# Kernel optimization log

Measured on AMD Instinct MI355X. Metric: run time of the kernel, lower is better.

Reference implementation:

```python
import jax, jax.numpy as jnp
import numpy as np

N_NODES = 100000
N_EDGES = 1200000
N_GRAPHS = 512
IN_DIM, HID, N_CLS = 16, 64, 2
EPS = 1e-5


def setup_inputs() -> dict:
    key = jax.random.key(0)
    ks = jax.random.split(key, 24)
    d = {}
    d["x"] = jax.random.normal(ks[0], (N_NODES, IN_DIM), dtype=jnp.float32)
    d["edge_index"] = jax.random.randint(ks[1], (2, N_EDGES), 0, N_NODES, dtype=jnp.int32)
    d["batch_ids"] = jnp.sort(jax.random.randint(ks[2], (N_NODES,), 0, N_GRAPHS, dtype=jnp.int32))
    # input batchnorm affine
    d["bn_in_g"] = jnp.ones((IN_DIM,), jnp.float32)
    d["bn_in_b"] = jnp.zeros((IN_DIM,), jnp.float32)
    # 3 GCN layers: weight, bias, bn gamma, bn beta
    dims = [(IN_DIM, HID), (HID, HID), (HID, HID)]
    for i, (ci, co) in enumerate(dims):
        s = 1.0 / np.sqrt(ci)
        d[f"W{i}"] = jax.random.uniform(ks[3 + 4 * i], (ci, co), jnp.float32, -s, s)
        d[f"b{i}"] = jnp.zeros((co,), jnp.float32)
        d[f"g{i}"] = jnp.ones((co,), jnp.float32)
        d[f"be{i}"] = jnp.zeros((co,), jnp.float32)
    # classifier head: Linear(HID,HID) -> ReLU -> Linear(HID,N_CLS)
    s = 1.0 / np.sqrt(HID)
    d["Wc1"] = jax.random.uniform(ks[20], (HID, HID), jnp.float32, -s, s)
    d["bc1"] = jax.random.uniform(ks[21], (HID,), jnp.float32, -s, s)
    d["Wc2"] = jax.random.uniform(ks[22], (HID, N_CLS), jnp.float32, -s, s)
    d["bc2"] = jax.random.uniform(ks[23], (N_CLS,), jnp.float32, -s, s)
    return d


def _batchnorm(x, g, b):
    # training-mode BatchNorm1d: biased batch stats over nodes
    m = jnp.mean(x, axis=0)
    v = jnp.mean(jnp.square(x - m), axis=0)
    return (x - m) * jax.lax.rsqrt(v + EPS) * g + b


def _gcn(x, W, b, src, dst, dis):
    # GCNConv: out[i] = sum_{j->i} dis[j]*dis[i] * (x_j W) + b  (self-loops included in src/dst)
    h = x @ W                                  # [N, co]
    msg = h[src] * (dis[src] * dis[dst])[:, None]  # [E+N, co] gather
    return jax.ops.segment_sum(msg, dst, num_segments=N_NODES) + b


def reference(x, bn_in_g, bn_in_b, W0, b0, g0, be0, W1, b1, g1, be1,
              W2, b2, g2, be2, Wc1, bc1, Wc2, bc2, edge_index, batch_ids):
    loops = jnp.arange(N_NODES, dtype=edge_index.dtype)
    src = jnp.concatenate([edge_index[0], loops])
    dst = jnp.concatenate([edge_index[1], loops])
    deg = jax.ops.segment_sum(jnp.ones(src.shape[0], x.dtype), dst, num_segments=N_NODES)
    dis = jnp.where(deg > 0, jax.lax.rsqrt(jnp.maximum(deg, 1e-12)), 0.0)

    h = _batchnorm(x, bn_in_g, bn_in_b)
    for W, b, g, be in ((W0, b0, g0, be0), (W1, b1, g1, be1), (W2, b2, g2, be2)):
        h = jax.nn.relu(_batchnorm(_gcn(h, W, b, src, dst, dis), g, be))

    # global mean pool over graphs
    sums = jax.ops.segment_sum(h, batch_ids, num_segments=N_GRAPHS)
    cnt = jax.ops.segment_sum(jnp.ones((N_NODES,), h.dtype), batch_ids, num_segments=N_GRAPHS)
    pooled = sums / jnp.maximum(cnt, 1.0)[:, None]

    # classifier head (dropout omitted: eval mode)
    z = jax.nn.relu(pooled @ Wc1 + bc1)
    return z @ Wc2 + bc2
```

## Files before the change

### kernel.cpp

```cpp
#include <hip/hip_runtime.h>
#include <hip/hip_bf16.h>

#define N_NODES 100000
#define N_EDGES 1200000
#define N_GRAPHS 512
#define HID 64
#define IN_DIM 16
#define EPS 1e-5f

#define NB_BUCKETS 391
#define BUCKET_SPAN 256
#define REGION 4096
#define BIN_TILE 4096
#define CSR_LEN (N_EDGES + N_NODES)
#define NREP 64
#define STATS_BLKS 64

typedef _Float16 half4 __attribute__((ext_vector_type(4)));
typedef _Float16 half8 __attribute__((ext_vector_type(8)));


__global__ void bin_stats_kernel(const int* __restrict__ ei, int* __restrict__ bucketCnt,
                                 int* __restrict__ regions, const float* __restrict__ x,
                                 float* __restrict__ sums, float* __restrict__ sumsq,
                                 _Float16* __restrict__ hwBuf, int nbBin) {
    __shared__ int hist[NB_BUCKETS], basem[NB_BUCKETS], cur[NB_BUCKETS];
    __shared__ float ls[16], lq[16];
    int t = threadIdx.x;

    if (blockIdx.x >= nbBin) {
        const int sblk = blockIdx.x - nbBin;
        if (sblk == 0 && t < 8)
            ((float4*)(hwBuf + (size_t)N_NODES * HID))[t] = make_float4(0.f, 0.f, 0.f, 0.f);
        if (t < 16) { ls[t] = 0.f; lq[t] = 0.f; }
        __syncthreads();
        const float4* x4 = (const float4*)x;
        const int total4 = N_NODES * IN_DIM / 4;
        float s0 = 0.f, s1 = 0.f, s2 = 0.f, s3 = 0.f;
        float q0 = 0.f, q1 = 0.f, q2 = 0.f, q3 = 0.f;
        int i = sblk * 256 + t;
        const int fb = (i & 3) * 4;
        for (; i < total4; i += STATS_BLKS * 256) {
            float4 v = x4[i];
            s0 += v.x; q0 += v.x * v.x;
            s1 += v.y; q1 += v.y * v.y;
            s2 += v.z; q2 += v.z * v.z;
            s3 += v.w; q3 += v.w * v.w;
        }
        atomicAdd(&ls[fb + 0], s0); atomicAdd(&lq[fb + 0], q0);
        atomicAdd(&ls[fb + 1], s1); atomicAdd(&lq[fb + 1], q1);
        atomicAdd(&ls[fb + 2], s2); atomicAdd(&lq[fb + 2], q2);
        atomicAdd(&ls[fb + 3], s3); atomicAdd(&lq[fb + 3], q3);
        __syncthreads();
        if (t < 16) { atomicAdd(&sums[t], ls[t]); atomicAdd(&sumsq[t], lq[t]); }
        return;
    }

    for (int i = t; i < NB_BUCKETS; i += 256) { hist[i] = 0; cur[i] = 0; }
    __syncthreads();
    const int4* ei4s = (const int4*)ei;
    const int4* ei4d = (const int4*)(ei + N_EDGES);
    int srcs[16], dsts[16];
#pragma unroll
    for (int i = 0; i < 4; i++) {
        int idx4 = blockIdx.x * (BIN_TILE / 4) + t + i * 256;
        if (idx4 * 4 < N_EDGES) {
            int4 s4 = ei4s[idx4];
            int4 d4 = ei4d[idx4];
            srcs[i * 4 + 0] = s4.x; dsts[i * 4 + 0] = d4.x;
            srcs[i * 4 + 1] = s4.y; dsts[i * 4 + 1] = d4.y;
            srcs[i * 4 + 2] = s4.z; dsts[i * 4 + 2] = d4.z;
            srcs[i * 4 + 3] = s4.w; dsts[i * 4 + 3] = d4.w;
            atomicAdd(&hist[d4.x >> 8], 1);
            atomicAdd(&hist[d4.y >> 8], 1);
            atomicAdd(&hist[d4.z >> 8], 1);
            atomicAdd(&hist[d4.w >> 8], 1);
        } else {
            dsts[i * 4 + 0] = -1; dsts[i * 4 + 1] = -1;
            dsts[i * 4 + 2] = -1; dsts[i * 4 + 3] = -1;
        }
    }
    __syncthreads();
    for (int i = t; i < NB_BUCKETS; i += 256) {
        int h = hist[i];
        basem[i] = h ? atomicAdd(&bucketCnt[i], h) : 0;
    }
    __syncthreads();
#pragma unroll
    for (int i = 0; i < 16; i++) {
        if (dsts[i] >= 0) {
            int b = dsts[i] >> 8;
            int pos = basem[b] + atomicAdd(&cur[b], 1);
            if (pos < REGION)
                regions[b * REGION + pos] = srcs[i] | ((dsts[i] & 255) << 17);
        }
    }
}


__global__ void build_kernel(const int* __restrict__ regions, const int* __restrict__ bucketCnt,
                             int* __restrict__ csrOff, int* __restrict__ csrSrc,
                             float* __restrict__ dis, const float* __restrict__ x,
                             const float* __restrict__ sums, const float* __restrict__ sumsq,
                             const float* __restrict__ gamma, const float* __restrict__ beta,
                             half4* __restrict__ m4) {
    __shared__ int deg[256], cur[256];
    __shared__ int slice[REGION + 256];
    __shared__ int wred1[4], wred2[4];
    __shared__ float sc16[16], sh16[16];
    int b = blockIdx.x, t = threadIdx.x;
    const int laneid = t & 63;
    const int w = t >> 6;

    if (t < 16) {
        const float invn = 1.0f / (float)N_NODES;
        float m = sums[t] * invn;
        float var = sumsq[t] * invn - m * m;
        float rs = rsqrtf(var + EPS);
        sc16[t] = gamma[t] * rs;
        sh16[t] = beta[t] - m * sc16[t];
    }
    {
        int s = 0;
        for (int i = t; i < NB_BUCKETS; i += 256)
            if (i < b) s += min(bucketCnt[i], REGION);
#pragma unroll
        for (int d = 1; d < 64; d <<= 1) s += __shfl_xor(s, d, 64);
        if (laneid == 0) wred1[w] = s;
    }
    int cnt = min(bucketCnt[b], REGION);
    int nbase = b * BUCKET_SPAN;
    int n = nbase + t;
    bool valid = (n < N_NODES);
    deg[t] = valid ? 1 : 0;
    __syncthreads();
    const int bb = wred1[0] + wred1[1] + wred1[2] + wred1[3] + b * BUCKET_SPAN;

    for (int i = t; i < cnt; i += 256) {
        int rec = regions[b * REGION + i];
        atomicAdd(&deg[rec >> 17], 1);
    }
    __syncthreads();
    int d = deg[t];

    int v = d;
#pragma unroll
    for (int sh = 1; sh < 64; sh <<= 1) {
        int u = __shfl_up(v, sh, 64);
        if (laneid >= sh) v += u;
    }
    if (laneid == 63) wred2[w] = v;
    __syncthreads();
    int wpre = 0;
#pragma unroll
    for (int ww = 0; ww < 4; ww++)
        if (ww < w) wpre += wred2[ww];
    const int tot = wred2[0] + wred2[1] + wred2[2] + wred2[3];
    int excl = v + wpre - d;

    float dv = rsqrtf((float)d);
    if (valid) {
        csrOff[n] = bb + excl;
        dis[n] = dv;
    }
    if (b == 0 && t == 0) csrOff[N_NODES] = CSR_LEN;
    cur[t] = excl;
    __syncthreads();
    if (valid) {
        int pos = atomicAdd(&cur[t], 1);
        slice[pos] = n;
    }
    for (int i = t; i < cnt; i += 256) {
        int rec = regions[b * REGION + i];
        int pos = atomicAdd(&cur[rec >> 17], 1);
        slice[pos] = rec & 0x1FFFF;
    }
    __syncthreads();
    for (int i = t; i < tot; i += 256) csrSrc[bb + i] = slice[i];

    if (valid) {
        const float4* xr = (const float4*)x + (size_t)n * 4;
        half4* mr = m4 + (size_t)n * 4;
#pragma unroll
        for (int c = 0; c < 4; c++) {
            float4 h = xr[c];
            half4 o;
            o.x = (_Float16)((h.x * sc16[c * 4 + 0] + sh16[c * 4 + 0]) * dv);
            o.y = (_Float16)((h.y * sc16[c * 4 + 1] + sh16[c * 4 + 1]) * dv);
            o.z = (_Float16)((h.z * sc16[c * 4 + 2] + sh16[c * 4 + 2]) * dv);
            o.w = (_Float16)((h.w * sc16[c * 4 + 3] + sh16[c * 4 + 3]) * dv);
            mr[c] = o;
        }
    } else if (n == N_NODES) {
        half4 z;
        z.x = (_Float16)0.f; z.y = (_Float16)0.f; z.z = (_Float16)0.f; z.w = (_Float16)0.f;
        half4* mr = m4 + (size_t)n * 4;
#pragma unroll
        for (int c = 0; c < 4; c++) mr[c] = z;
    }
}


__device__ __forceinline__ void bn_coef_rep(const float* rep, const float* gamma,
                                            const float* beta, int k, float& sc, float& sh) {
    float S = 0.f, Q = 0.f;
    for (int r = 0; r < NREP; r++) { S += rep[r * 128 + k]; Q += rep[r * 128 + 64 + k]; }
    const float invn = 1.0f / (float)N_NODES;
    float m = S * invn;
    float var = Q * invn - m * m;
    float rs = rsqrtf(var + EPS);
    sc = gamma[k] * rs;
    sh = beta[k] - m * sc;
}


__global__ void agg16_gemm0_kernel(const half4* __restrict__ m4, const int* __restrict__ csrOff,
                                   const int* __restrict__ csrSrc, const float* __restrict__ dis,
                                   const float* __restrict__ W, const float* __restrict__ bias,
                                   _Float16* __restrict__ y, float* __restrict__ statsRep) {
    const int t = threadIdx.x;
    const int lane = t & 63;
    const int wid = t >> 6;
    const int g = lane >> 4;
    const int s = lane & 15;
    const int fl = s & 3;
    const int q = s >> 2;
    const int wave = blockIdx.x * 4 + wid;
    const int nwaves = gridDim.x * 4;

    float wreg[16][4];
#pragma unroll
    for (int k = 0; k < 16; k++) {
#pragma unroll
        for (int j = 0; j < 4; j++) wreg[k][j] = W[k * HID + s + 16 * j];
    }
    float bj[4];
#pragma unroll
    for (int j = 0; j < 4; j++) bj[j] = bias[s + 16 * j];
    float sv[4] = {0.f, 0.f, 0.f, 0.f}, qv[4] = {0.f, 0.f, 0.f, 0.f};

    for (int n0 = wave * 4; n0 < N_NODES; n0 += nwaves * 4) {
        int n = n0 + g;
        bool vn = (n < N_NODES);
        int beg = 0, end = 0;
        if (vn) { beg = csrOff[n]; end = csrOff[n + 1]; }
        float4 acc = make_float4(0.f, 0.f, 0.f, 0.f);
        int e = beg + q;
        int i0 = (e < end) ? csrSrc[e] : N_NODES;
        int i1 = (e + 4 < end) ? csrSrc[e + 4] : N_NODES;
        while (e < end) {
            int j0 = i0, j1 = i1;
            e += 8;
            i0 = (e < end) ? csrSrc[e] : N_NODES;
            i1 = (e + 4 < end) ? csrSrc[e + 4] : N_NODES;
            half4 v0 = m4[(size_t)j0 * 4 + fl];
            half4 v1 = m4[(size_t)j1 * 4 + fl];
            acc.x += (float)v0.x + (float)v1.x;
            acc.y += (float)v0.y + (float)v1.y;
            acc.z += (float)v0.z + (float)v1.z;
            acc.w += (float)v0.w + (float)v1.w;
        }
        acc.x += __shfl_xor(acc.x, 4, 64);  acc.y += __shfl_xor(acc.y, 4, 64);
        acc.z += __shfl_xor(acc.z, 4, 64);  acc.w += __shfl_xor(acc.w, 4, 64);
        acc.x += __shfl_xor(acc.x, 8, 64);  acc.y += __shfl_xor(acc.y, 8, 64);
        acc.z += __shfl_xor(acc.z, 8, 64);  acc.w += __shfl_xor(acc.w, 8, 64);
        float d = vn ? dis[n] : 0.f;
        acc.x *= d; acc.y *= d; acc.z *= d; acc.w *= d;
        float yv0 = bj[0], yv1 = bj[1], yv2 = bj[2], yv3 = bj[3];
        const int gbase = lane & 48;
#pragma unroll
        for (int k = 0; k < 16; k++) {
            float comp = ((k & 3) == 0) ? acc.x : ((k & 3) == 1) ? acc.y
                        : ((k & 3) == 2) ? acc.z : acc.w;
            float a = __shfl(comp, gbase + (k >> 2), 64);
            yv0 += a * wreg[k][0];
            yv1 += a * wreg[k][1];
            yv2 += a * wreg[k][2];
            yv3 += a * wreg[k][3];
        }
        if (vn) {
            _Float16* yr = y + (size_t)n * HID;
            yr[s] = (_Float16)yv0; yr[s + 16] = (_Float16)yv1;
            yr[s + 32] = (_Float16)yv2; yr[s + 48] = (_Float16)yv3;
            sv[0] += yv0; qv[0] += yv0 * yv0;
            sv[1] += yv1; qv[1] += yv1 * yv1;
            sv[2] += yv2; qv[2] += yv2 * yv2;
            sv[3] += yv3; qv[3] += yv3 * yv3;
        }
    }
#pragma unroll
    for (int j = 0; j < 4; j++) {
        sv[j] += __shfl_xor(sv[j], 16, 64); sv[j] += __shfl_xor(sv[j], 32, 64);
        qv[j] += __shfl_xor(qv[j], 16, 64); qv[j] += __shfl_xor(qv[j], 32, 64);
    }
    __shared__ float ls[4][64], lq[4][64];
    if (g == 0) {
#pragma unroll
        for (int j = 0; j < 4; j++) { ls[wid][s + 16 * j] = sv[j]; lq[wid][s + 16 * j] = qv[j]; }
    }
    __syncthreads();
    if (wid == 0) {
        float S = ls[0][lane] + ls[1][lane] + ls[2][lane] + ls[3][lane];
        float Q = lq[0][lane] + lq[1][lane] + lq[2][lane] + lq[3][lane];
        float* rep = statsRep + (blockIdx.x & (NREP - 1)) * 128;
        atomicAdd(&rep[lane], S);
        atomicAdd(&rep[64 + lane], Q);
    }
}


#define G64_ROWS 128
__global__ void gemm64_kernel(const _Float16* __restrict__ hin, const float* __restrict__ W,
                              const float* __restrict__ statsRep, const float* __restrict__ gamma,
                              const float* __restrict__ beta, const float* __restrict__ dis,
                              _Float16* __restrict__ hout) {
    __shared__ float Ws[HID * HID];
    __shared__ float hs[G64_ROWS][HID + 2];
    __shared__ float scb[64], shb[64];
    int t = threadIdx.x;
    int fg = t & 15;
    int rg = t >> 4;
    int base = blockIdx.x * G64_ROWS;

    if (t < 64) bn_coef_rep(statsRep, gamma, beta, t, scb[t], shb[t]);
    {
        const float4* W4 = (const float4*)W;
        float4* Ws4 = (float4*)Ws;
        for (int i = t; i < HID * HID / 4; i += 256) Ws4[i] = W4[i];
    }
    __syncthreads();
    {
        const half4* hin4 = (const half4*)hin;
        for (int i = t; i < G64_ROWS * 16; i += 256) {
            int r = i >> 4, c = i & 15;
            int n = base + r;
            float4 v = make_float4(0.f, 0.f, 0.f, 0.f);
            if (n < N_NODES) {
                half4 h = hin4[n * 16 + c];
                v.x = fmaxf((float)h.x * scb[c * 4 + 0] + shb[c * 4 + 0], 0.f);
                v.y = fmaxf((float)h.y * scb[c * 4 + 1] + shb[c * 4 + 1], 0.f);
                v.z = fmaxf((float)h.z * scb[c * 4 + 2] + shb[c * 4 + 2], 0.f);
                v.w = fmaxf((float)h.w * scb[c * 4 + 3] + shb[c * 4 + 3], 0.f);
            }
            hs[r][c * 4 + 0] = v.x;
            hs[r][c * 4 + 1] = v.y;
            hs[r][c * 4 + 2] = v.z;
            hs[r][c * 4 + 3] = v.w;
        }
    }
    __syncthreads();

    float4 acc[8];
#pragma unroll
    for (int r = 0; r < 8; r++) acc[r] = make_float4(0.f, 0.f, 0.f, 0.f);
    const float4* Ws4 = (const float4*)Ws;
    for (int k = 0; k < HID; k += 2) {
        float4 wk0 = Ws4[k * 16 + fg];
        float4 wk1 = Ws4[(k + 1) * 16 + fg];
#pragma unroll
        for (int r = 0; r < 8; r++) {
            float2 h2 = *(const float2*)&hs[rg * 8 + r][k];
            acc[r].x += h2.x * wk0.x + h2.y * wk1.x;
            acc[r].y += h2.x * wk0.y + h2.y * wk1.y;
            acc[r].z += h2.x * wk0.z + h2.y * wk1.z;
            acc[r].w += h2.x * wk0.w + h2.y * wk1.w;
        }
    }
    half4* hout4 = (half4*)hout;
#pragma unroll
    for (int r = 0; r < 8; r++) {
        int n = base + rg * 8 + r;
        if (n < N_NODES) {
            float dsc = dis[n];
            half4 o;
            o.x = (_Float16)(acc[r].x * dsc);
            o.y = (_Float16)(acc[r].y * dsc);
            o.z = (_Float16)(acc[r].z * dsc);
            o.w = (_Float16)(acc[r].w * dsc);
            hout4[n * 16 + fg] = o;
        }
    }
}


__global__ void aggregate_kernel(const half8* __restrict__ hwh, const int* __restrict__ csrOff,
                                 const int* __restrict__ csrSrc, const float* __restrict__ dis,
                                 const float* __restrict__ bias, half8* __restrict__ y8,
                                 float* __restrict__ statsRep) {
    const int lane = threadIdx.x & 63;
    const int wid = threadIdx.x >> 6;
    const int g = lane >> 5;
    const int s = lane & 31;
    const int c = s & 7;
    const int o = s >> 3;
    const int wave = blockIdx.x * 4 + wid;
    const int nwaves = gridDim.x * 4;

    const float4 bv0 = ((const float4*)bias)[c * 2];
    const float4 bv1 = ((const float4*)bias)[c * 2 + 1];
    float sa[8], qa[8];
#pragma unroll
    for (int j = 0; j < 8; j++) { sa[j] = 0.f; qa[j] = 0.f; }

    for (int n0 = wave * 2; n0 < N_NODES; n0 += nwaves * 2) {
        int n = n0 + g;
        bool vn = (n < N_NODES);
        int beg = 0, end = 0;
        if (vn) { beg = csrOff[n]; end = csrOff[n + 1]; }
        float acc[8];
#pragma unroll
        for (int j = 0; j < 8; j++) acc[j] = 0.f;
        int e = beg + o;
        int i0 = (e < end) ? csrSrc[e] : N_NODES;
        int i1 = (e + 4 < end) ? csrSrc[e + 4] : N_NODES;
        while (e < end) {
            int j0 = i0, j1 = i1;
            e += 8;
            i0 = (e < end) ? csrSrc[e] : N_NODES;
            i1 = (e + 4 < end) ? csrSrc[e + 4] : N_NODES;
            half8 h0 = hwh[(size_t)j0 * 8 + c];
            half8 h1 = hwh[(size_t)j1 * 8 + c];
#pragma unroll
            for (int j = 0; j < 8; j++) acc[j] += (float)h0[j] + (float)h1[j];
        }
#pragma unroll
        for (int j = 0; j < 8; j++) {
            acc[j] += __shfl_xor(acc[j], 8, 64);
            acc[j] += __shfl_xor(acc[j], 16, 64);
        }
        if (o == 0 && vn) {
            float d = dis[n];
            float val[8];
            val[0] = acc[0] * d + bv0.x; val[1] = acc[1] * d + bv0.y;
            val[2] = acc[2] * d + bv0.z; val[3] = acc[3] * d + bv0.w;
            val[4] = acc[4] * d + bv1.x; val[5] = acc[5] * d + bv1.y;
            val[6] = acc[6] * d + bv1.z; val[7] = acc[7] * d + bv1.w;
            half8 ov;
#pragma unroll
            for (int j = 0; j < 8; j++) ov[j] = (_Float16)val[j];
            y8[(size_t)n * 8 + c] = ov;
#pragma unroll
            for (int j = 0; j < 8; j++) { sa[j] += val[j]; qa[j] += val[j] * val[j]; }
        }
    }
#pragma unroll
    for (int j = 0; j < 8; j++) {
        sa[j] += __shfl_xor(sa[j], 32, 64);
        qa[j] += __shfl_xor(qa[j], 32, 64);
    }
    __shared__ float ls[4][64], lq[4][64];
    ls[wid][lane] = 0.f;
    lq[wid][lane] = 0.f;
    if (lane < 8) {
#pragma unroll
        for (int j = 0; j < 8; j++) { ls[wid][lane * 8 + j] = sa[j]; lq[wid][lane * 8 + j] = qa[j]; }
    }
    __syncthreads();
    if (wid == 0) {
        float S = ls[0][lane] + ls[1][lane] + ls[2][lane] + ls[3][lane];
        float Q = lq[0][lane] + lq[1][lane] + lq[2][lane] + lq[3][lane];
        float* rep = statsRep + (blockIdx.x & (NREP - 1)) * 128;
        atomicAdd(&rep[lane], S);
        atomicAdd(&rep[64 + lane], Q);
    }
}


#define POOL_CHUNK 256
__global__ void pool_kernel(const _Float16* __restrict__ y, const int* __restrict__ batch,
                            const float* __restrict__ statsRep, const float* __restrict__ gamma,
                            const float* __restrict__ beta, float* __restrict__ pool,
                            float* __restrict__ cnt) {
    __shared__ float scs[64], shs[64];
    int t = threadIdx.x;
    int f = t & 63;
    int nl = t >> 6;
    if (t < 64) bn_coef_rep(statsRep, gamma, beta, t, scs[t], shs[t]);
    __syncthreads();
    float sc = scs[f], sh = shs[f];
    int base = blockIdx.x * POOL_CHUNK;
    int endn = min(base + POOL_CHUNK, N_NODES);
    int g_cur = -1;
    float acc = 0.f;
    float c_acc = 0.f;
    for (int n = base + nl; n < endn; n += 4) {
        int g = batch[n];
        float v = fmaxf((float)y[(size_t)n * HID + f] * sc + sh, 0.f);
        if (g != g_cur) {
            if (g_cur >= 0) {
                atomicAdd(&pool[g_cur * HID + f], acc);
                if (f == 0) atomicAdd(&cnt[g_cur], c_acc);
            }
            g_cur = g;
            acc = 0.f;
            c_acc = 0.f;
        }
        acc += v;
        c_acc += 1.f;
    }
    if (g_cur >= 0) {
        atomicAdd(&pool[g_cur * HID + f], acc);
        if (f == 0) atomicAdd(&cnt[g_cur], c_acc);
    }
}

__global__ void head_kernel(const float* __restrict__ pool, const float* __restrict__ cnt,
                            const float* __restrict__ Wc1, const float* __restrict__ bc1,
                            const float* __restrict__ Wc2, const float* __restrict__ bc2,
                            float* __restrict__ out) {
    int g = blockIdx.x;
    int f = threadIdx.x;
    __shared__ float p[64], z[64];
    float c = fmaxf(cnt[g], 1.0f);
    p[f] = pool[g * HID + f] / c;
    __syncthreads();
    float acc = bc1[f];
    for (int k = 0; k < 64; k++) acc += p[k] * Wc1[k * 64 + f];
    z[f] = fmaxf(acc, 0.f);
    __syncthreads();
    if (f < 2) {
        float o = bc2[f];
        for (int k = 0; k < 64; k++) o += z[k] * Wc2[k * 2 + f];
        out[g * 2 + f] = o;
    }
}


extern "C" void kernel_launch(void* const* d_in, const int* in_sizes, int n_in,
                              void* d_out, int out_size, void* d_ws, size_t ws_size,
                              hipStream_t stream) {
    const float* x      = (const float*)d_in[0];
    const int*   ei     = (const int*)d_in[1];
    const int*   batch  = (const int*)d_in[2];
    const float* bn_in_g = (const float*)d_in[3];
    const float* bn_in_b = (const float*)d_in[4];
    const float* W0 = (const float*)d_in[5];
    const float* b0 = (const float*)d_in[6];
    const float* g0 = (const float*)d_in[7];
    const float* be0 = (const float*)d_in[8];
    const float* W1 = (const float*)d_in[9];
    const float* b1 = (const float*)d_in[10];
    const float* g1 = (const float*)d_in[11];
    const float* be1 = (const float*)d_in[12];
    const float* W2 = (const float*)d_in[13];
    const float* b2 = (const float*)d_in[14];
    const float* g2 = (const float*)d_in[15];
    const float* be2 = (const float*)d_in[16];
    const float* Wc1 = (const float*)d_in[17];
    const float* bc1 = (const float*)d_in[18];
    const float* Wc2 = (const float*)d_in[19];
    const float* bc2 = (const float*)d_in[20];
    float* out = (float*)d_out;

    char* w = (char*)d_ws;
    size_t off = 0;
    auto take = [&](size_t bytes) {
        size_t r = off;
        off += (bytes + 255) & ~(size_t)255;
        return r;
    };
    float* stats    = (float*)(w + take(256 * 4));
    float* statsRep = (float*)(w + take(3 * NREP * 128 * 4));
    float* pool     = (float*)(w + take((size_t)N_GRAPHS * HID * 4));
    float* cnt      = (float*)(w + take((size_t)N_GRAPHS * 4));
    int* bucketCnt  = (int*)(w + take((size_t)NB_BUCKETS * 4));
    size_t zero_end = off;
    float* dis    = (float*)(w + take((size_t)N_NODES * 4));
    int* csrOff   = (int*)(w + take((size_t)(N_NODES + 1) * 4));
    int* csrSrc   = (int*)(w + take((size_t)(CSR_LEN + 64) * 4));
    _Float16* hwBuf = (_Float16*)(w + take((size_t)(N_NODES + 1) * HID * 2));
    _Float16* yBuf  = (_Float16*)(w + take((size_t)N_NODES * HID * 2));
    _Float16* msgBuf = (_Float16*)(w + take((size_t)(N_NODES + 1) * IN_DIM * 2));
    int* regions  = (int*)hwBuf;
    (void)ws_size; (void)n_in; (void)in_sizes; (void)out_size;

    hipMemsetAsync(w, 0, zero_end, stream);

    const int nbBin   = (N_EDGES + BIN_TILE - 1) / BIN_TILE;
    const int nbG64   = (N_NODES + G64_ROWS - 1) / G64_ROWS;
    const int nbAgg16 = (N_NODES + 16 * 4 - 1) / (16 * 4);
    const int nbAgg64 = (N_NODES + 8 * 4 - 1) / (8 * 4);

    float* s0 = stats;
    float* rep1 = statsRep + 0 * NREP * 128;
    float* rep2 = statsRep + 1 * NREP * 128;
    float* rep3 = statsRep + 2 * NREP * 128;

    bin_stats_kernel<<<nbBin + STATS_BLKS, 256, 0, stream>>>(ei, bucketCnt, regions, x, s0,
                                                             s0 + 64, hwBuf, nbBin);
    build_kernel<<<NB_BUCKETS, 256, 0, stream>>>(regions, bucketCnt, csrOff, csrSrc, dis, x,
                                                 s0, s0 + 64, bn_in_g, bn_in_b,
                                                 (half4*)msgBuf);

    agg16_gemm0_kernel<<<nbAgg16, 256, 0, stream>>>((const half4*)msgBuf, csrOff, csrSrc, dis,
                                                    W0, b0, yBuf, rep1);

    gemm64_kernel<<<nbG64, 256, 0, stream>>>(yBuf, W1, rep1, g0, be0, dis, hwBuf);
    aggregate_kernel<<<nbAgg64, 256, 0, stream>>>((const half8*)hwBuf, csrOff, csrSrc, dis, b1,
                                                  (half8*)yBuf, rep2);
    gemm64_kernel<<<nbG64, 256, 0, stream>>>(yBuf, W2, rep2, g1, be1, dis, hwBuf);
    aggregate_kernel<<<nbAgg64, 256, 0, stream>>>((const half8*)hwBuf, csrOff, csrSrc, dis, b2,
                                                  (half8*)yBuf, rep3);

    const int nbPool = (N_NODES + POOL_CHUNK - 1) / POOL_CHUNK;
    pool_kernel<<<nbPool, 256, 0, stream>>>(yBuf, batch, rep3, g2, be2, pool, cnt);
    head_kernel<<<N_GRAPHS, 64, 0, stream>>>(pool, cnt, Wc1, bc1, Wc2, bc2, out);
}
```

Measured before the change: 304.2 us.

## Fuse mean pooling and classifier head into one per-graph kernel

Replaces the atomic-based pooling kernel and the separate head kernel with one kernel that runs one block per graph. Each block finds its node range in the sorted batch ids by binary search, reduces the normalized ReLU features in shared memory, and then applies the MLP head directly. This removes a kernel launch, the global atomics, and the pool/count buffers along with their zeroing. In exchange, parallelism drops to 512 blocks, each scanning about 200 nodes, and the kernel relies on batch_ids being sorted.

```diff
diff --git a/kernel.cpp b/kernel.cpp
--- a/kernel.cpp
+++ b/kernel.cpp
@@ -466,62 +466,51 @@
 }
 
 
-#define POOL_CHUNK 256
-__global__ void pool_kernel(const _Float16* __restrict__ y, const int* __restrict__ batch,
-                            const float* __restrict__ statsRep, const float* __restrict__ gamma,
-                            const float* __restrict__ beta, float* __restrict__ pool,
-                            float* __restrict__ cnt) {
+__global__ void pool_head_kernel(const _Float16* __restrict__ y, const int* __restrict__ batch,
+                                 const float* __restrict__ statsRep,
+                                 const float* __restrict__ gamma, const float* __restrict__ beta,
+                                 const float* __restrict__ Wc1, const float* __restrict__ bc1,
+                                 const float* __restrict__ Wc2, const float* __restrict__ bc2,
+                                 float* __restrict__ out) {
     __shared__ float scs[64], shs[64];
-    int t = threadIdx.x;
-    int f = t & 63;
-    int nl = t >> 6;
+    __shared__ float sm[4][64];
+    __shared__ float p[64], z[64];
+    const int g = blockIdx.x;
+    const int t = threadIdx.x;
+    const int f = t & 63;
+    const int nl = t >> 6;
+
     if (t < 64) bn_coef_rep(statsRep, gamma, beta, t, scs[t], shs[t]);
-    __syncthreads();
-    float sc = scs[f], sh = shs[f];
-    int base = blockIdx.x * POOL_CHUNK;
-    int endn = min(base + POOL_CHUNK, N_NODES);
-    int g_cur = -1;
-    float acc = 0.f;
-    float c_acc = 0.f;
-    for (int n = base + nl; n < endn; n += 4) {
-        int g = batch[n];
-        float v = fmaxf((float)y[(size_t)n * HID + f] * sc + sh, 0.f);
-        if (g != g_cur) {
-            if (g_cur >= 0) {
-                atomicAdd(&pool[g_cur * HID + f], acc);
-                if (f == 0) atomicAdd(&cnt[g_cur], c_acc);
-            }
-            g_cur = g;
-            acc = 0.f;
-            c_acc = 0.f;
-        }
-        acc += v;
-        c_acc += 1.f;
-    }
-    if (g_cur >= 0) {
-        atomicAdd(&pool[g_cur * HID + f], acc);
-        if (f == 0) atomicAdd(&cnt[g_cur], c_acc);
-    }
-}
-
-__global__ void head_kernel(const float* __restrict__ pool, const float* __restrict__ cnt,
-                            const float* __restrict__ Wc1, const float* __restrict__ bc1,
-                            const float* __restrict__ Wc2, const float* __restrict__ bc2,
-                            float* __restrict__ out) {
-    int g = blockIdx.x;
-    int f = threadIdx.x;
-    __shared__ float p[64], z[64];
-    float c = fmaxf(cnt[g], 1.0f);
-    p[f] = pool[g * HID + f] / c;
-    __syncthreads();
-    float acc = bc1[f];
-    for (int k = 0; k < 64; k++) acc += p[k] * Wc1[k * 64 + f];
-    z[f] = fmaxf(acc, 0.f);
-    __syncthreads();
-    if (f < 2) {
-        float o = bc2[f];
-        for (int k = 0; k < 64; k++) o += z[k] * Wc2[k * 2 + f];
-        out[g * 2 + f] = o;
+
+    int lo = 0, hi = N_NODES;
+    while (lo < hi) { int m = (lo + hi) >> 1; if (batch[m] < g) lo = m + 1; else hi = m; }
+    const int start = lo;
+    hi = N_NODES;
+    while (lo < hi) { int m = (lo + hi) >> 1; if (batch[m] < g + 1) lo = m + 1; else hi = m; }
+    const int end = lo;
+    __syncthreads();
+
+    const float sc = scs[f], sh = shs[f];
+    float a = 0.f;
+    for (int n = start + nl; n < end; n += 4)
+        a += fmaxf((float)y[(size_t)n * HID + f] * sc + sh, 0.f);
+    sm[nl][f] = a;
+    __syncthreads();
+    if (t < 64) {
+        float c = fmaxf((float)(end - start), 1.0f);
+        p[t] = (sm[0][t] + sm[1][t] + sm[2][t] + sm[3][t]) / c;
+    }
+    __syncthreads();
+    if (t < 64) {
+        float acc = bc1[t];
+        for (int k = 0; k < 64; k++) acc += p[k] * Wc1[k * 64 + t];
+        z[t] = fmaxf(acc, 0.f);
+    }
+    __syncthreads();
+    if (t < 2) {
+        float o = bc2[t];
+        for (int k = 0; k < 64; k++) o += z[k] * Wc2[k * 2 + t];
+        out[g * 2 + t] = o;
     }
 }
 
@@ -561,8 +550,6 @@
     };
     float* stats    = (float*)(w + take(256 * 4));
     float* statsRep = (float*)(w + take(3 * NREP * 128 * 4));
-    float* pool     = (float*)(w + take((size_t)N_GRAPHS * HID * 4));
-    float* cnt      = (float*)(w + take((size_t)N_GRAPHS * 4));
     int* bucketCnt  = (int*)(w + take((size_t)NB_BUCKETS * 4));
     size_t zero_end = off;
     float* dis    = (float*)(w + take((size_t)N_NODES * 4));
@@ -602,7 +589,6 @@
     aggregate_kernel<<<nbAgg64, 256, 0, stream>>>((const half8*)hwBuf, csrOff, csrSrc, dis, b2,
                                                   (half8*)yBuf, rep3);
 
-    const int nbPool = (N_NODES + POOL_CHUNK - 1) / POOL_CHUNK;
-    pool_kernel<<<nbPool, 256, 0, stream>>>(yBuf, batch, rep3, g2, be2, pool, cnt);
-    head_kernel<<<N_GRAPHS, 64, 0, stream>>>(pool, cnt, Wc1, bc1, Wc2, bc2, out);
-}
+    pool_head_kernel<<<N_GRAPHS, 256, 0, stream>>>(yBuf, batch, rep3, g2, be2,
+                                                   Wc1, bc1, Wc2, bc2, out);
+}
```

After: 305.0 us. No clear change (+0.3%).
